# Performance work log

Measured on AMD Instinct MI355X. Metric: run time of the kernel, lower is better.

Reference implementation:

```python
import jax, jax.numpy as jnp
import numpy as np

NBINS = 256  # skimage threshold_otsu default
SMOOTH = 1.0


def _otsu_threshold(x):
    """Otsu threshold of a flat float array, skimage-style 256-bin histogram."""
    x = x.reshape(-1)
    xmin = x.min()
    xmax = x.max()
    span = xmax - xmin
    scale = jnp.where(span > 0, NBINS / span, 0.0)
    idx = jnp.clip(((x - xmin) * scale).astype(jnp.int32), 0, NBINS - 1)
    hist = jnp.zeros(NBINS, dtype=x.dtype).at[idx].add(1.0)
    centers = xmin + (jnp.arange(NBINS, dtype=x.dtype) + 0.5) * (span / NBINS)
    # class weights and means (first bin always contains min, last contains max,
    # so the cumulative sums used below are strictly positive)
    w1 = jnp.cumsum(hist)
    w2 = jnp.cumsum(hist[::-1])
    m1 = jnp.cumsum(hist * centers) / w1
    m2 = (jnp.cumsum((hist * centers)[::-1]) / w2)[::-1]
    w2 = w2[::-1]
    var12 = w1[:-1] * w2[1:] * (m1[:-1] - m2[1:]) ** 2  # inter-class variance
    return centers[jnp.argmax(var12)]


def setup_inputs() -> dict:
    key = jax.random.key(0)
    k1, k2 = jax.random.split(key)
    B, C, H, W = 64, 1, 512, 512
    output = jax.random.normal(k1, (B, C, H, W), dtype=jnp.float32)
    target = (jax.random.uniform(k2, (B, C, H, W)) > 0.5).astype(jnp.float32)
    return {"output": output, "target": target}


def reference(output, target):
    probs = jax.nn.sigmoid(output)                    # [B,C,H,W]
    thresh = jax.vmap(_otsu_threshold)(probs)         # per-sample Otsu, [B]
    binary = (probs > thresh[:, None, None, None]).astype(probs.dtype)
    intersection = (binary * target).sum(axis=(-1, -2))          # [B,C]
    union = (binary + target).sum(axis=(-1, -2)) - intersection  # [B,C]
    iou = (intersection + SMOOTH) / (union + SMOOTH)
    return iou.mean()  # reduction='mean'
```

## Files before the change

### kernel.cpp

```cpp
#include <hip/hip_runtime.h>
#include <cstdint>

static constexpr int BATCH = 64;
static constexpr int NPB   = 512 * 512;
static constexpr int NFB   = 2048;
static constexpr int PBLK  = 8;
static constexpr int ELB   = NPB / PBLK;

static constexpr int W_BMIN = 0;
static constexpr int W_BMAX = 512;
static constexpr int W_PART = 1024;

__device__ __forceinline__ float sigmoidf(float v) {
  if (v >= 0.0f) return 1.0f / (1.0f + expf(-v));
  float e = expf(v);
  return e / (1.0f + e);
}
__device__ __forceinline__ float fsig(float v) {
  return __builtin_amdgcn_rcpf(1.0f + __expf(-v));
}

__global__ __launch_bounds__(256) void k_pass(const float* __restrict__ x,
                                              const float* __restrict__ tg,
                                              uint32_t* __restrict__ ws,
                                              float* __restrict__ out) {
  __shared__ uint32_t h[2 * 2 * NFB];
  const int t = threadIdx.x;
  const int g = blockIdx.x;
  if (g == 0 && t == 0) out[0] = 0.0f;
  const uint4 z = {0u, 0u, 0u, 0u};
#pragma unroll
  for (int j = 0; j < 8; ++j) reinterpret_cast<uint4*>(h)[t + j * 256] = z;
  __syncthreads();

  const int b = g >> 3;
  const int blk = g & 7;
  const size_t base = (size_t)b * NPB + (size_t)blk * ELB;
  const float4* px = reinterpret_cast<const float4*>(x + base);
  const float4* pt = reinterpret_cast<const float4*>(tg + base);
  const uint32_t woff = (uint32_t)(t >> 7) << 12;

  float mn = INFINITY, mx = -INFINITY;
#pragma unroll 4
  for (int i = 0; i < 32; ++i) {
    float4 v = px[i * 256 + t];
    float4 w = pt[i * 256 + t];
    mn = fminf(mn, fminf(fminf(v.x, v.y), fminf(v.z, v.w)));
    mx = fmaxf(mx, fmaxf(fmaxf(v.x, v.y), fmaxf(v.z, v.w)));
#define PUT(a, c) { int idx = (int)(fsig(a) * 2048.0f);                   \
                    idx = idx > 2047 ? 2047 : idx;                        \
                    idx += ((c) > 0.5f) ? 2048 : 0;                       \
                    atomicAdd(&h[woff + idx], 1u); }
    PUT(v.x, w.x) PUT(v.y, w.y) PUT(v.z, w.z) PUT(v.w, w.w)
#undef PUT
  }
  for (int off = 32; off; off >>= 1) {
    mn = fminf(mn, __shfl_down(mn, off));
    mx = fmaxf(mx, __shfl_down(mx, off));
  }
  __shared__ float smn[4], smx[4];
  if ((t & 63) == 0) { smn[t >> 6] = mn; smx[t >> 6] = mx; }
  __syncthreads();
  if (t == 0) {
    float* wsf = reinterpret_cast<float*>(ws);
    wsf[W_BMIN + g] = fminf(fminf(smn[0], smn[1]), fminf(smn[2], smn[3]));
    wsf[W_BMAX + g] = fmaxf(fmaxf(smx[0], smx[1]), fmaxf(smx[2], smx[3]));
  }
  uint32_t* gp = ws + W_PART + (size_t)g * (2 * NFB / 2);
#pragma unroll
  for (int j = 0; j < 8; ++j) {
    const int w = t + j * 256;
    const uint32_t c0 = h[2 * w] + h[2 * w + 4096];
    const uint32_t c1 = h[2 * w + 1] + h[2 * w + 1 + 4096];
    gp[w] = c0 | (c1 << 16);
  }
}

__global__ __launch_bounds__(256) void k_finalize(uint32_t* __restrict__ ws,
                                                  float* __restrict__ out) {
  __shared__ uint32_t fj[2 * NFB];
  __shared__ uint32_t h256[256];
  __shared__ uint32_t w1s[256];
  __shared__ float s1s[256];
  __shared__ float vv[256];
  __shared__ int vi[256];
  __shared__ unsigned long long redL[256];
  __shared__ float sPmin, sScale, sBinw;
  const int b = blockIdx.x;
  const int t = threadIdx.x;
  const float* wsf = reinterpret_cast<const float*>(ws);

#pragma unroll
  for (int j = 0; j < 8; ++j) {
    const int w = t + j * 256;
    uint32_t a0 = 0, a1 = 0;
#pragma unroll
    for (int p = 0; p < PBLK; ++p) {
      const uint32_t v = ws[W_PART + (size_t)(b * PBLK + p) * NFB + w];
      a0 += v & 0xFFFFu;
      a1 += v >> 16;
    }
    fj[2 * w] = a0;
    fj[2 * w + 1] = a1;
  }
  h256[t] = 0u;
  float mnv = (t < PBLK) ? wsf[W_BMIN + b * PBLK + t] : INFINITY;
  float mxv = (t < PBLK) ? wsf[W_BMAX + b * PBLK + t] : -INFINITY;
  for (int off = 4; off; off >>= 1) {
    mnv = fminf(mnv, __shfl_down(mnv, off));
    mxv = fmaxf(mxv, __shfl_down(mxv, off));
  }
  if (t == 0) {
    const float pmin = sigmoidf(mnv);
    const float pmax = sigmoidf(mxv);
    const float span = pmax - pmin;
    sPmin = pmin;
    sScale = (span > 0.0f) ? (512.0f / span) : 0.0f;
    sBinw = span * (1.0f / 256.0f);
  }
  __syncthreads();
  const float pmin = sPmin, scale = sScale, binw = sBinw;

#define CIDX(k) ({ const float rep = ((float)(k) + 0.5f) * (1.0f / 2048.0f);  \
                   int ci = (int)((rep - pmin) * scale);                      \
                   ci = ci < 0 ? 0 : (ci > 511 ? 511 : ci); ci; })
#pragma unroll
  for (int j = 0; j < 8; ++j) {
    const int w = t + j * 256;
    const int i0 = 2 * w, i1 = 2 * w + 1;
    const int k0 = i0 & (NFB - 1), k1 = i1 & (NFB - 1);
    if (fj[i0]) atomicAdd(&h256[CIDX(k0) >> 1], fj[i0]);
    if (fj[i1]) atomicAdd(&h256[CIDX(k1) >> 1], fj[i1]);
  }
  __syncthreads();

  const uint32_t hk = h256[t];
  const float ck = pmin + ((float)t + 0.5f) * binw;
  w1s[t] = hk;
  s1s[t] = (float)hk * ck;
  for (int off = 1; off < 256; off <<= 1) {
    __syncthreads();
    uint32_t wp = (t >= off) ? w1s[t - off] : 0u;
    float    sp = (t >= off) ? s1s[t - off] : 0.0f;
    __syncthreads();
    w1s[t] += wp; s1s[t] += sp;
  }
  __syncthreads();
  const uint32_t totW = w1s[255];
  const float totS = s1s[255];
  float v = -INFINITY;
  if (t < 255 && w1s[t] > 0u && totW > w1s[t]) {
    const float w1f = (float)w1s[t];
    const float w2f = (float)(totW - w1s[t]);
    const float m1 = s1s[t] / w1f;
    const float m2 = (totS - s1s[t]) / w2f;
    const float d = m1 - m2;
    v = (w1f * w2f) * (d * d);
  }
  vv[t] = v; vi[t] = t;
  for (int s = 128; s; s >>= 1) {
    __syncthreads();
    if (t < s) {
      const float vb = vv[t + s]; const int ib = vi[t + s];
      if (vb > vv[t] || (vb == vv[t] && ib < vi[t])) { vv[t] = vb; vi[t] = ib; }
    }
  }
  __syncthreads();
  const int J = 2 * vi[0] + 1;

  uint32_t nb_p = 0, ni_p = 0, nt_p = 0;
#pragma unroll
  for (int j = 0; j < 8; ++j) {
    const int w = t + j * 256;
#pragma unroll
    for (int e = 0; e < 2; ++e) {
      const int idx = 2 * w + e;
      const uint32_t cnt = fj[idx];
      const int cls = idx >> 11;
      const int k = idx & (NFB - 1);
      nt_p += cls ? cnt : 0u;
      if (CIDX(k) >= J) { nb_p += cnt; ni_p += cls ? cnt : 0u; }
    }
  }
#undef CIDX
  redL[t] = (unsigned long long)nb_p | ((unsigned long long)ni_p << 20) | ((unsigned long long)nt_p << 40);
  for (int s = 128; s; s >>= 1) {
    __syncthreads();
    if (t < s) redL[t] += redL[t + s];
  }
  __syncthreads();
  if (t == 0) {
    const unsigned long long P = redL[0];
    const float nb = (float)(uint32_t)(P & 0xFFFFFu);
    const float ni = (float)(uint32_t)((P >> 20) & 0xFFFFFu);
    const float nt = (float)(uint32_t)((P >> 40) & 0xFFFFFu);
    const float uni = nb + nt - ni;
    const float iou = (ni + 1.0f) / (uni + 1.0f);
    atomicAdd(out, iou * (1.0f / 64.0f));
  }
}

extern "C" void kernel_launch(void* const* d_in, const int* in_sizes, int n_in,
                              void* d_out, int out_size, void* d_ws, size_t ws_size,
                              hipStream_t stream) {
  const float* x  = (const float*)d_in[0];
  const float* tg = (const float*)d_in[1];
  uint32_t* ws = (uint32_t*)d_ws;
  float* out = (float*)d_out;

  hipLaunchKernelGGL(k_pass,     dim3(BATCH * PBLK), dim3(256), 0, stream, x, tg, ws, out);
  hipLaunchKernelGGL(k_finalize, dim3(BATCH),        dim3(256), 0, stream, ws, out);
}
```

Before: 33.68 us.

## Split each sample across more blocks, chosen by available workspace size

The pass kernel is templated on the number of blocks per sample (32, 16 or 8), picked at launch from the workspace size. This spreads the streaming histogram work over more workgroups to fill the GPU better. The duplicated per-half-block shared histograms are dropped to halve LDS use, and per-wave min/max values are written straight to global memory without a block-level reduction. The cost is more partial histograms for finalize to merge and more shared-atomic contention on a single histogram copy. The 16-bit packed counts still fit because each block now handles fewer elements.

After: 39.02 us. 15.9% more time.

```diff
diff --git a/kernel.cpp b/kernel.cpp
--- a/kernel.cpp
+++ b/kernel.cpp
@@ -4,12 +4,10 @@
 static constexpr int BATCH = 64;
 static constexpr int NPB   = 512 * 512;
 static constexpr int NFB   = 2048;
-static constexpr int PBLK  = 8;
-static constexpr int ELB   = NPB / PBLK;
 
 static constexpr int W_BMIN = 0;
-static constexpr int W_BMAX = 512;
-static constexpr int W_PART = 1024;
+static constexpr int W_BMAX = 8192;
+static constexpr int W_PART = 16384;
 
 __device__ __forceinline__ float sigmoidf(float v) {
   if (v >= 0.0f) return 1.0f / (1.0f + expf(-v));
@@ -20,29 +18,31 @@
   return __builtin_amdgcn_rcpf(1.0f + __expf(-v));
 }
 
+template <int PBLK>
 __global__ __launch_bounds__(256) void k_pass(const float* __restrict__ x,
                                               const float* __restrict__ tg,
                                               uint32_t* __restrict__ ws,
                                               float* __restrict__ out) {
-  __shared__ uint32_t h[2 * 2 * NFB];
+  constexpr int ELB  = NPB / PBLK;
+  constexpr int ITER = ELB / 4 / 256;
+  __shared__ uint32_t h[2 * NFB];
   const int t = threadIdx.x;
   const int g = blockIdx.x;
   if (g == 0 && t == 0) out[0] = 0.0f;
-  const uint4 z = {0u, 0u, 0u, 0u};
-#pragma unroll
-  for (int j = 0; j < 8; ++j) reinterpret_cast<uint4*>(h)[t + j * 256] = z;
-  __syncthreads();
-
-  const int b = g >> 3;
-  const int blk = g & 7;
+#pragma unroll
+  for (int j = 0; j < 4; ++j)
+    reinterpret_cast<uint4*>(h)[t + j * 256] = uint4{0u, 0u, 0u, 0u};
+  __syncthreads();
+
+  const int b = g / PBLK;
+  const int blk = g % PBLK;
   const size_t base = (size_t)b * NPB + (size_t)blk * ELB;
   const float4* px = reinterpret_cast<const float4*>(x + base);
   const float4* pt = reinterpret_cast<const float4*>(tg + base);
-  const uint32_t woff = (uint32_t)(t >> 7) << 12;
 
   float mn = INFINITY, mx = -INFINITY;
 #pragma unroll 4
-  for (int i = 0; i < 32; ++i) {
+  for (int i = 0; i < ITER; ++i) {
     float4 v = px[i * 256 + t];
     float4 w = pt[i * 256 + t];
     mn = fminf(mn, fminf(fminf(v.x, v.y), fminf(v.z, v.w)));
@@ -50,7 +50,7 @@
 #define PUT(a, c) { int idx = (int)(fsig(a) * 2048.0f);                   \
                     idx = idx > 2047 ? 2047 : idx;                        \
                     idx += ((c) > 0.5f) ? 2048 : 0;                       \
-                    atomicAdd(&h[woff + idx], 1u); }
+                    atomicAdd(&h[idx], 1u); }
     PUT(v.x, w.x) PUT(v.y, w.y) PUT(v.z, w.z) PUT(v.w, w.w)
 #undef PUT
   }
@@ -58,24 +58,21 @@
     mn = fminf(mn, __shfl_down(mn, off));
     mx = fmaxf(mx, __shfl_down(mx, off));
   }
-  __shared__ float smn[4], smx[4];
-  if ((t & 63) == 0) { smn[t >> 6] = mn; smx[t >> 6] = mx; }
-  __syncthreads();
-  if (t == 0) {
+  if ((t & 63) == 0) {
     float* wsf = reinterpret_cast<float*>(ws);
-    wsf[W_BMIN + g] = fminf(fminf(smn[0], smn[1]), fminf(smn[2], smn[3]));
-    wsf[W_BMAX + g] = fmaxf(fmaxf(smx[0], smx[1]), fmaxf(smx[2], smx[3]));
-  }
-  uint32_t* gp = ws + W_PART + (size_t)g * (2 * NFB / 2);
-#pragma unroll
-  for (int j = 0; j < 8; ++j) {
-    const int w = t + j * 256;
-    const uint32_t c0 = h[2 * w] + h[2 * w + 4096];
-    const uint32_t c1 = h[2 * w + 1] + h[2 * w + 1 + 4096];
-    gp[w] = c0 | (c1 << 16);
-  }
-}
-
+    wsf[W_BMIN + g * 4 + (t >> 6)] = mn;
+    wsf[W_BMAX + g * 4 + (t >> 6)] = mx;
+  }
+  __syncthreads();
+  uint32_t* gp = ws + W_PART + (size_t)g * NFB;
+#pragma unroll
+  for (int j = 0; j < 8; ++j) {
+    const int w = t + j * 256;
+    gp[w] = h[2 * w] | (h[2 * w + 1] << 16);
+  }
+}
+
+template <int PBLK>
 __global__ __launch_bounds__(256) void k_finalize(uint32_t* __restrict__ ws,
                                                   float* __restrict__ out) {
   __shared__ uint32_t fj[2 * NFB];
@@ -94,7 +91,6 @@
   for (int j = 0; j < 8; ++j) {
     const int w = t + j * 256;
     uint32_t a0 = 0, a1 = 0;
-#pragma unroll
     for (int p = 0; p < PBLK; ++p) {
       const uint32_t v = ws[W_PART + (size_t)(b * PBLK + p) * NFB + w];
       a0 += v & 0xFFFFu;
@@ -104,19 +100,24 @@
     fj[2 * w + 1] = a1;
   }
   h256[t] = 0u;
-  float mnv = (t < PBLK) ? wsf[W_BMIN + b * PBLK + t] : INFINITY;
-  float mxv = (t < PBLK) ? wsf[W_BMAX + b * PBLK + t] : -INFINITY;
-  for (int off = 4; off; off >>= 1) {
-    mnv = fminf(mnv, __shfl_down(mnv, off));
-    mxv = fmaxf(mxv, __shfl_down(mxv, off));
-  }
-  if (t == 0) {
-    const float pmin = sigmoidf(mnv);
-    const float pmax = sigmoidf(mxv);
-    const float span = pmax - pmin;
-    sPmin = pmin;
-    sScale = (span > 0.0f) ? (512.0f / span) : 0.0f;
-    sBinw = span * (1.0f / 256.0f);
+  if (t < 64) {
+    float mnv = INFINITY, mxv = -INFINITY;
+    for (int i = t; i < PBLK * 4; i += 64) {
+      mnv = fminf(mnv, wsf[W_BMIN + b * PBLK * 4 + i]);
+      mxv = fmaxf(mxv, wsf[W_BMAX + b * PBLK * 4 + i]);
+    }
+    for (int off = 32; off; off >>= 1) {
+      mnv = fminf(mnv, __shfl_down(mnv, off));
+      mxv = fmaxf(mxv, __shfl_down(mxv, off));
+    }
+    if (t == 0) {
+      const float pmin = sigmoidf(mnv);
+      const float pmax = sigmoidf(mxv);
+      const float span = pmax - pmin;
+      sPmin = pmin;
+      sScale = (span > 0.0f) ? (512.0f / span) : 0.0f;
+      sBinw = span * (1.0f / 256.0f);
+    }
   }
   __syncthreads();
   const float pmin = sPmin, scale = sScale, binw = sBinw;
@@ -200,6 +201,13 @@
   }
 }
 
+template <int PBLK>
+static void launch_all(const float* x, const float* tg, uint32_t* ws, float* out,
+                       hipStream_t stream) {
+  hipLaunchKernelGGL((k_pass<PBLK>),     dim3(BATCH * PBLK), dim3(256), 0, stream, x, tg, ws, out);
+  hipLaunchKernelGGL((k_finalize<PBLK>), dim3(BATCH),        dim3(256), 0, stream, ws, out);
+}
+
 extern "C" void kernel_launch(void* const* d_in, const int* in_sizes, int n_in,
                               void* d_out, int out_size, void* d_ws, size_t ws_size,
                               hipStream_t stream) {
@@ -208,6 +216,9 @@
   uint32_t* ws = (uint32_t*)d_ws;
   float* out = (float*)d_out;
 
-  hipLaunchKernelGGL(k_pass,     dim3(BATCH * PBLK), dim3(256), 0, stream, x, tg, ws, out);
-  hipLaunchKernelGGL(k_finalize, dim3(BATCH),        dim3(256), 0, stream, ws, out);
-}
+  const size_t need32 = (size_t)(W_PART + BATCH * 32 * NFB) * 4;
+  const size_t need16 = (size_t)(W_PART + BATCH * 16 * NFB) * 4;
+  if (ws_size >= need32)      launch_all<32>(x, tg, ws, out, stream);
+  else if (ws_size >= need16) launch_all<16>(x, tg, ws, out, stream);
+  else                        launch_all<8>(x, tg, ws, out, stream);
+}
```
